# Kernel tuning notes

Hardware: AMD Instinct MI355X
Metric: run time of the kernel (lower is better)

The kernel has to match this reference:

```python
import jax, jax.numpy as jnp
import numpy as np

B, T, N, D, C = 32, 256, 256, 1024, 80
SIM_THRESH = 0.7
MAX_AGE = 10
W_SIM, W_IOU = 0.7, 0.3


def setup_inputs() -> dict:
    key = jax.random.key(0)
    ks = jax.random.split(key, 8)
    track_memory = jax.random.normal(ks[0], (B, T, D), jnp.float32)
    track_boxes = jax.random.uniform(ks[1], (B, T, 4), jnp.float32, 0.05, 0.95)
    track_active = jax.random.bernoulli(ks[2], 0.9, (B, T))
    track_age = jax.random.randint(ks[3], (B, T), 0, 5, jnp.int32)
    track_hits = jax.random.randint(ks[4], (B, T), 1, 10, jnp.int32)
    det_boxes = jax.random.uniform(ks[5], (B, N, 4), jnp.float32, 0.05, 0.95)
    # correlate detections with tracks so cosine similarity exceeds the
    # matching threshold for many pairs and the greedy loop does real work
    det_memory = track_memory + 0.3 * jax.random.normal(ks[6], (B, N, D), jnp.float32)
    class_logits = jax.random.normal(ks[7], (B, N, C), jnp.float32)
    return {
        'track_memory': track_memory, 'track_boxes': track_boxes,
        'track_active': track_active, 'track_age': track_age,
        'track_hits': track_hits, 'det_boxes': det_boxes,
        'det_memory': det_memory, 'class_logits': class_logits,
    }


def _normalize(x):
    # matches F.normalize(dim=-1): x / max(||x||, eps)
    n = jnp.linalg.norm(x, axis=-1, keepdims=True)
    return x / jnp.maximum(n, 1e-12)


def _iou_matrix(tb, db):
    # tb [T,4], db [N,4], boxes in (cx, cy, w, h) format -> IoU [T,N]
    t_x1, t_y1 = tb[:, 0] - tb[:, 2] / 2, tb[:, 1] - tb[:, 3] / 2
    t_x2, t_y2 = tb[:, 0] + tb[:, 2] / 2, tb[:, 1] + tb[:, 3] / 2
    d_x1, d_y1 = db[:, 0] - db[:, 2] / 2, db[:, 1] - db[:, 3] / 2
    d_x2, d_y2 = db[:, 0] + db[:, 2] / 2, db[:, 1] + db[:, 3] / 2
    iw = jnp.clip(jnp.minimum(t_x2[:, None], d_x2[None, :]) - jnp.maximum(t_x1[:, None], d_x1[None, :]), 0.0)
    ih = jnp.clip(jnp.minimum(t_y2[:, None], d_y2[None, :]) - jnp.maximum(t_y1[:, None], d_y1[None, :]), 0.0)
    inter = iw * ih
    union = (tb[:, 2] * tb[:, 3])[:, None] + (db[:, 2] * db[:, 3])[None, :] - inter
    return inter / (union + 1e-6)


def _greedy_match(Cmat):
    # sequential greedy argmax matching, as in the torch while-loop.
    # returns match_det [T]: detection index matched to each track, -1 if none.
    Tn, Nn = Cmat.shape

    def step(carry, _):
        Cm, match_det = carry
        flat = Cm.reshape(-1)
        idx = jnp.argmax(flat)
        val = flat[idx]
        ok = val >= SIM_THRESH
        t = idx // Nn
        d = idx % Nn
        match_det = jnp.where(ok, match_det.at[t].set(d.astype(jnp.int32)), match_det)
        Cm = jnp.where(ok, Cm.at[t, :].set(-1.0).at[:, d].set(-1.0), Cm)
        return (Cm, match_det), None

    init = (Cmat, jnp.full((Tn,), -1, jnp.int32))
    (_, match_det), _ = jax.lax.scan(step, init, None, length=min(Tn, Nn))
    return match_det


def reference(track_memory, track_boxes, track_active, track_age, track_hits,
              det_boxes, det_memory, class_logits):
    # detection scores (computed in torch update(); not used downstream)
    scores = jnp.max(jax.nn.softmax(class_logits, axis=-1), axis=-1)  # [B,N]

    def per_batch(tm, tb, ta, age, hits, db, dm):
        sim = _normalize(tm) @ _normalize(dm).T            # [T,N] cosine sim
        iou = _iou_matrix(tb, db)                          # [T,N]
        Cmat = W_SIM * sim + W_IOU * iou
        Cmat = jnp.where(ta[:, None], Cmat, -1.0)          # inactive rows -> -1
        match_det = _greedy_match(Cmat)                    # [T]
        matched = match_det >= 0
        d = jnp.clip(match_det, 0)
        new_mem = jnp.where(matched[:, None], dm[d], tm)
        new_box = jnp.where(matched[:, None], db[d], tb)
        new_hits = jnp.where(matched, hits + 1, hits)
        unmatched_active = ta & ~matched
        new_age = jnp.where(matched, 0, jnp.where(unmatched_active, age + 1, age))
        new_active = jnp.where(matched, True,
                               jnp.where(unmatched_active, new_age <= MAX_AGE, ta))
        return new_mem, new_box, new_active, new_age, new_hits, match_det

    new_mem, new_box, new_active, new_age, new_hits, match_det = jax.vmap(per_batch)(
        track_memory, track_boxes, track_active, track_age, track_hits,
        det_boxes, det_memory)
    return new_mem, new_box, new_active, new_age, new_hits, match_det, scores
```

## Files before the change

kernel.cpp:

```cpp
#include <hip/hip_runtime.h>
#include <math.h>

static constexpr int PB = 32, PT = 256, PN = 256, PD = 1024, PC = 80;
static constexpr int BCAP = 96;
static constexpr int CAP  = 256;
static constexpr int NT   = 16;

static constexpr size_t O_MEM   = 0;
static constexpr size_t O_BOX   = O_MEM   + (size_t)PB*PT*PD;
static constexpr size_t O_ACT   = O_BOX   + (size_t)PB*PT*4;
static constexpr size_t O_AGE   = O_ACT   + (size_t)PB*PT;
static constexpr size_t O_HITS  = O_AGE   + (size_t)PB*PT;
static constexpr size_t O_MATCH = O_HITS  + (size_t)PB*PT;
static constexpr size_t O_SCORE = O_MATCH + (size_t)PB*PT;

typedef __attribute__((ext_vector_type(8))) short short8;
typedef __attribute__((ext_vector_type(4))) float f32x4;


__device__ __forceinline__ unsigned ordbits(float f) {
    unsigned b = __float_as_uint(f);
    return (b & 0x80000000u) ? ~b : (b | 0x80000000u);
}
__device__ __forceinline__ unsigned short f2bf(float f) {
    unsigned u = __float_as_uint(f);
    unsigned r = u + 0x7fffu + ((u >> 16) & 1u);
    return (unsigned short)(r >> 16);
}
__device__ __forceinline__ short8 pack8(float4 lo, float4 hi) {
    union { unsigned u[4]; short8 s; } r;
    r.u[0] = f2bf(lo.x) | ((unsigned)f2bf(lo.y) << 16);
    r.u[1] = f2bf(lo.z) | ((unsigned)f2bf(lo.w) << 16);
    r.u[2] = f2bf(hi.x) | ((unsigned)f2bf(hi.y) << 16);
    r.u[3] = f2bf(hi.z) | ((unsigned)f2bf(hi.w) << 16);
    return r.s;
}

__device__ __forceinline__ float box_cost(float sim, float4 bt, float4 bd) {
    float tX1 = bt.x - bt.z*0.5f, tX2 = bt.x + bt.z*0.5f;
    float tY1 = bt.y - bt.w*0.5f, tY2 = bt.y + bt.w*0.5f;
    float dX1 = bd.x - bd.z*0.5f, dX2 = bd.x + bd.z*0.5f;
    float dY1 = bd.y - bd.w*0.5f, dY2 = bd.y + bd.w*0.5f;
    float iw = fmaxf(fminf(tX2, dX2) - fmaxf(tX1, dX1), 0.f);
    float ih = fmaxf(fminf(tY2, dY2) - fmaxf(tY1, dY1), 0.f);
    float inter = iw * ih;
    float iou = inter / (bt.z*bt.w + bd.z*bd.w - inter + 1e-6f);
    return 0.7f * sim + 0.3f * iou;
}

__global__ __launch_bounds__(512) void k_prep(
        const float* __restrict__ tm, const float* __restrict__ dm,
        const float* __restrict__ lg,
        short* __restrict__ abf, short* __restrict__ bbf,
        float* __restrict__ asums, float* __restrict__ bsums,
        float* __restrict__ ddots, float* __restrict__ out) {
    const int bx = blockIdx.x;
    const int tid = threadIdx.x;
    const int w = tid >> 6, lane = tid & 63;
    if (bx < PB * PT / 16) {
        const int m16 = lane & 15, quad = lane >> 4;
        const int row = bx * 16 + m16;
        const float* tp = tm + (size_t)row * PD;
        const float* dp = dm + (size_t)row * PD;
        const size_t fb = (size_t)bx * 32 * 512;
        float as = 0.f, bs = 0.f, dd = 0.f;
#pragma unroll
        for (int kq = 0; kq < 4; ++kq) {
            const int kk = w * 4 + kq;
            const int e = kk * 32 + quad * 8;
            float4 a0 = *(const float4*)(tp + e);
            float4 a1 = *(const float4*)(tp + e + 4);
            float4 d0 = *(const float4*)(dp + e);
            float4 d1 = *(const float4*)(dp + e + 4);
            as += a0.x*a0.x + a0.y*a0.y + a0.z*a0.z + a0.w*a0.w
                + a1.x*a1.x + a1.y*a1.y + a1.z*a1.z + a1.w*a1.w;
            bs += d0.x*d0.x + d0.y*d0.y + d0.z*d0.z + d0.w*d0.w
                + d1.x*d1.x + d1.y*d1.y + d1.z*d1.z + d1.w*d1.w;
            dd += a0.x*d0.x + a0.y*d0.y + a0.z*d0.z + a0.w*d0.w
                + a1.x*d1.x + a1.y*d1.y + a1.z*d1.z + a1.w*d1.w;
            *(short8*)(abf + fb + (size_t)kk * 512 + lane * 8) = pack8(a0, a1);
            *(short8*)(bbf + fb + (size_t)kk * 512 + lane * 8) = pack8(d0, d1);
        }
        as += __shfl_xor(as, 16); as += __shfl_xor(as, 32);
        bs += __shfl_xor(bs, 16); bs += __shfl_xor(bs, 32);
        dd += __shfl_xor(dd, 16); dd += __shfl_xor(dd, 32);
        __shared__ float red[3][8][16];
        if (quad == 0) { red[0][w][m16] = as; red[1][w][m16] = bs; red[2][w][m16] = dd; }
        __syncthreads();
        if (tid < 16) {
            int rg = bx * 16 + tid;
            float s0 = 0.f, s1 = 0.f, s2 = 0.f;
#pragma unroll
            for (int j = 0; j < 8; ++j) {
                s0 += red[0][j][tid]; s1 += red[1][j][tid]; s2 += red[2][j][tid];
            }
            asums[rg] = s0; bsums[rg] = s1; ddots[rg] = s2;
        }
    } else {
        int rowi = (bx - PB * PT / 16) * 8 + w;
        const float* p = lg + (size_t)rowi * PC;
        float x0 = p[lane];
        float x1 = (lane < PC - 64) ? p[64 + lane] : -INFINITY;
        float m = fmaxf(x0, x1);
#pragma unroll
        for (int o = 32; o > 0; o >>= 1) m = fmaxf(m, __shfl_down(m, o));
        m = __shfl(m, 0);
        float s = expf(x0 - m) + ((lane < PC - 64) ? expf(x1 - m) : 0.f);
#pragma unroll
        for (int o = 32; o > 0; o >>= 1) s += __shfl_down(s, o);
        if (lane == 0) out[O_SCORE + rowi] = 1.0f / s;
    }
}

__global__ __launch_bounds__(512) void k_sim(
        const short* __restrict__ abf, const short* __restrict__ bbf,
        const float* __restrict__ tb, const float* __restrict__ db,
        const unsigned* __restrict__ ta,
        const float* __restrict__ asums, const float* __restrict__ bsums,
        unsigned* __restrict__ cntblk, int* __restrict__ cand) {
    const int i = blockIdx.x;
    const int xcd = i & 7, j = i >> 3;
    const int b = xcd * 4 + (j >> 4);
    const int tile = j & 15;
    const int rowbase = (tile >> 2) * 64;
    const int colbase = (tile & 3) * 64;
    const int bid = b * NT + tile;
    const int tid = threadIdx.x;
    const int w = tid >> 6, lane = tid & 63;
    const int wm = w & 3, wn = w >> 2;
    const int m16 = lane & 15, quad = lane >> 4;

    __shared__ unsigned bcnt;
    __shared__ float ainv[64], binv[64];
    if (tid == 0) bcnt = 0u;
    if (tid < 64)
        ainv[tid] = 1.0f / fmaxf(sqrtf(asums[b * PT + rowbase + tid]), 1e-12f);
    else if (tid < 128)
        binv[tid - 64] = 1.0f / fmaxf(sqrtf(bsums[b * PN + colbase + tid - 64]), 1e-12f);

    const short8* A8 = (const short8*)abf;
    const short8* B8 = (const short8*)bbf;
    const size_t ab = ((size_t)(b * 16 + (rowbase >> 4) + wm)) * 2048 + lane;
    const size_t bbse = ((size_t)(b * 16 + (colbase >> 4) + wn * 2)) * 2048 + lane;

    f32x4 acc0 = (f32x4)0.f, acc1 = (f32x4)0.f;
    short8 av  = A8[ab];
    short8 b0v = B8[bbse];
    short8 b1v = B8[bbse + 2048];
#pragma unroll
    for (int kk = 0; kk < 31; ++kk) {
        const size_t o = (size_t)(kk + 1) * 64;
        short8 na  = A8[ab + o];
        short8 nb0 = B8[bbse + o];
        short8 nb1 = B8[bbse + o + 2048];
        acc0 = __builtin_amdgcn_mfma_f32_16x16x32_bf16(av, b0v, acc0, 0, 0, 0);
        acc1 = __builtin_amdgcn_mfma_f32_16x16x32_bf16(av, b1v, acc1, 0, 0, 0);
        av = na; b0v = nb0; b1v = nb1;
    }
    acc0 = __builtin_amdgcn_mfma_f32_16x16x32_bf16(av, b0v, acc0, 0, 0, 0);
    acc1 = __builtin_amdgcn_mfma_f32_16x16x32_bf16(av, b1v, acc1, 0, 0, 0);

    __syncthreads();

    float dx1[2], dy1[2], dx2[2], dy2[2], darea[2], dnv[2];
    int ng[2];
#pragma unroll
    for (int nj = 0; nj < 2; ++nj) {
        int cl = wn * 32 + nj * 16 + m16;
        ng[nj] = colbase + cl;
        dnv[nj] = binv[cl];
        float4 bx = *(const float4*)&db[((size_t)b * PN + ng[nj]) * 4];
        dx1[nj] = bx.x - bx.z * 0.5f; dx2[nj] = bx.x + bx.z * 0.5f;
        dy1[nj] = bx.y - bx.w * 0.5f; dy2[nj] = bx.y + bx.w * 0.5f;
        darea[nj] = bx.z * bx.w;
    }

#pragma unroll
    for (int r = 0; r < 4; ++r) {
        int tl = wm * 16 + quad * 4 + r;
        int tg = rowbase + tl;
        if (ta[b * PT + tg] == 0u) continue;
        float tnv = ainv[tl];
        float4 bx = *(const float4*)&tb[((size_t)b * PT + tg) * 4];
        float tX1 = bx.x - bx.z * 0.5f, tX2 = bx.x + bx.z * 0.5f;
        float tY1 = bx.y - bx.w * 0.5f, tY2 = bx.y + bx.w * 0.5f;
        float tA = bx.z * bx.w;
#pragma unroll
        for (int nj = 0; nj < 2; ++nj) {
            float sim = (nj == 0 ? acc0[r] : acc1[r]) * tnv * dnv[nj];
            float iw = fmaxf(fminf(tX2, dx2[nj]) - fmaxf(tX1, dx1[nj]), 0.f);
            float ih = fmaxf(fminf(tY2, dy2[nj]) - fmaxf(tY1, dy1[nj]), 0.f);
            float inter = iw * ih;
            float iou = inter / (tA + darea[nj] - inter + 1e-6f);
            float cost = 0.7f * sim + 0.3f * iou;
            if (cost >= 0.695f) {
                unsigned idx = atomicAdd(&bcnt, 1u);
                if (idx < BCAP) cand[bid * BCAP + idx] = (tg << 8) | ng[nj];
            }
        }
    }
    __syncthreads();
    if (tid == 0) cntblk[bid] = (bcnt > BCAP) ? BCAP : bcnt;
}

__global__ __launch_bounds__(512) void k_match(
        const float* __restrict__ tm, const float* __restrict__ dm,
        const float* __restrict__ tb, const float* __restrict__ db,
        const float* __restrict__ asums, const float* __restrict__ bsums,
        const float* __restrict__ ddots,
        const unsigned* __restrict__ cntblk, const int* __restrict__ cand,
        int* __restrict__ md) {
    const int b = blockIdx.x;
    const int tid = threadIdx.x;
    const int w = tid >> 6, lane = tid & 63;
    __shared__ int cnts[NT];
    __shared__ unsigned long long sel_key[CAP];
    __shared__ unsigned sel_cnt;
    __shared__ int odd_slot[64];
    __shared__ unsigned odd_cnt;
    __shared__ int rcnt[PT];
    __shared__ int ccnt[PN];
    __shared__ int conflict;

    if (tid == 0) { sel_cnt = 0u; odd_cnt = 0u; conflict = 0; }
    if (tid < NT) {
        int cj = (int)cntblk[b * NT + tid];
        cnts[tid] = (cj > BCAP) ? BCAP : cj;
    }
    if (tid < PT) { rcnt[tid] = 0; md[b * PT + tid] = -1; }
    if (tid < PN) ccnt[tid] = 0;
    __syncthreads();

    for (int u = tid; u < NT * BCAP; u += 512) {
        int j = u / BCAP, i = u - j * BCAP;
        if (i >= cnts[j]) continue;
        int gidx = (b * NT + j) * BCAP + i;
        int pair = cand[gidx];
        int t = pair >> 8, n = pair & 255;
        if (t == n) {
            float na  = asums[b * PT + t];
            float nb  = bsums[b * PN + n];
            float dot = ddots[b * PT + t];
            float sim = dot * (1.0f / fmaxf(sqrtf(na), 1e-12f))
                            * (1.0f / fmaxf(sqrtf(nb), 1e-12f));
            float4 bt = *(const float4*)&tb[((size_t)b * PT + t) * 4];
            float4 bd = *(const float4*)&db[((size_t)b * PN + n) * 4];
            float cost = box_cost(sim, bt, bd);
            if (cost >= 0.7f) {
                unsigned s = atomicAdd(&sel_cnt, 1u);
                if (s < CAP)
                    sel_key[s] = ((unsigned long long)ordbits(cost) << 16)
                               | (unsigned long long)(65535 - pair);
            }
        } else {
            unsigned oi = atomicAdd(&odd_cnt, 1u);
            if (oi < 64) odd_slot[oi] = gidx;
        }
    }
    __syncthreads();

    int nodd = (int)odd_cnt; if (nodd > 64) nodd = 64;
    for (int j = w; j < nodd; j += 8) {
        int pair = cand[odd_slot[j]];
        int t = pair >> 8, n = pair & 255;
        const float4* tr = (const float4*)(tm + ((size_t)b * PT + t) * PD);
        const float4* dr = (const float4*)(dm + ((size_t)b * PN + n) * PD);
        float dot = 0.f;
#pragma unroll
        for (int q = 0; q < 4; ++q) {
            float4 v = tr[lane + 64 * q];
            float4 u = dr[lane + 64 * q];
            dot += v.x*u.x + v.y*u.y + v.z*u.z + v.w*u.w;
        }
#pragma unroll
        for (int o = 1; o < 64; o <<= 1) dot += __shfl_xor(dot, o);
        if (lane == 0) {
            float na = asums[b * PT + t], nb = bsums[b * PN + n];
            float sim = dot * (1.0f / fmaxf(sqrtf(na), 1e-12f))
                            * (1.0f / fmaxf(sqrtf(nb), 1e-12f));
            float4 bt = *(const float4*)&tb[((size_t)b * PT + t) * 4];
            float4 bd = *(const float4*)&db[((size_t)b * PN + n) * 4];
            float cost = box_cost(sim, bt, bd);
            if (cost >= 0.7f) {
                unsigned s = atomicAdd(&sel_cnt, 1u);
                if (s < CAP)
                    sel_key[s] = ((unsigned long long)ordbits(cost) << 16)
                               | (unsigned long long)(65535 - pair);
            }
        }
    }
    __syncthreads();

    const unsigned ns = (sel_cnt > (unsigned)CAP) ? (unsigned)CAP : sel_cnt;
    for (unsigned s = tid; s < ns; s += 512) {
        int flat = 65535 - (int)(sel_key[s] & 0xFFFFull);
        if (atomicAdd(&rcnt[flat >> 8], 1) >= 1) conflict = 1;
        if (atomicAdd(&ccnt[flat & 255], 1) >= 1) conflict = 1;
    }
    __syncthreads();

    if (!conflict) {
        for (unsigned s = tid; s < ns; s += 512) {
            int flat = 65535 - (int)(sel_key[s] & 0xFFFFull);
            md[b * PT + (flat >> 8)] = flat & 255;
        }
        return;
    }

    if (w == 0) {
        unsigned long long k[4];
#pragma unroll
        for (int s = 0; s < 4; ++s) {
            unsigned idx = (unsigned)lane + 64u * s;
            k[s] = (idx < ns) ? sel_key[idx] : 0ull;
        }
        int mdv[4] = {-1, -1, -1, -1};
        for (int it = 0; it < PT; ++it) {
            unsigned long long m = k[0];
            if (k[1] > m) m = k[1];
            if (k[2] > m) m = k[2];
            if (k[3] > m) m = k[3];
#pragma unroll
            for (int o = 1; o < 64; o <<= 1) {
                unsigned long long s = __shfl_xor(m, o);
                if (s > m) m = s;
            }
            if (m == 0ull) break;
            int flat = 65535 - (int)(m & 0xFFFFull);
            int t = flat >> 8, d = flat & 255;
            if ((t & 63) == lane) mdv[t >> 6] = d;
#pragma unroll
            for (int s = 0; s < 4; ++s) {
                if (k[s]) {
                    int f2 = 65535 - (int)(k[s] & 0xFFFFull);
                    if ((f2 >> 8) == t || (f2 & 255) == d) k[s] = 0ull;
                }
            }
        }
#pragma unroll
        for (int s = 0; s < 4; ++s) md[b * PT + s * 64 + lane] = mdv[s];
    }
}

__global__ __launch_bounds__(256) void k_outsc(
        const float* __restrict__ tm, const float* __restrict__ tb,
        const unsigned* __restrict__ ta, const int* __restrict__ age,
        const int* __restrict__ hits, const float* __restrict__ db,
        const float* __restrict__ dm, const int* __restrict__ md,
        float* __restrict__ out) {
    const int w = threadIdx.x >> 6, lane = threadIdx.x & 63;
    int idx = blockIdx.x * 4 + w;
    int b = idx >> 8;
    int m = md[idx];
    bool matched = m >= 0;
    int d = matched ? m : 0;
    const float4* src = (const float4*)(matched ? dm + ((size_t)b * PN + d) * PD
                                                : tm + (size_t)idx * PD);
    float4* dst = (float4*)(out + O_MEM + (size_t)idx * PD);
#pragma unroll
    for (int q = 0; q < 4; ++q) dst[lane + 64 * q] = src[lane + 64 * q];
    if (lane < 4) {
        const float* sb = matched ? db + ((size_t)b * PN + d) * 4
                                  : tb + (size_t)idx * 4;
        out[O_BOX + (size_t)idx * 4 + lane] = sb[lane];
    }
    if (lane == 0) {
        bool tact = ta[idx] != 0u;
        int hh = hits[idx], ag = age[idx];
        int nh = matched ? hh + 1 : hh;
        bool unm = tact && !matched;
        int na = matched ? 0 : (unm ? ag + 1 : ag);
        bool nact = matched ? true : (unm ? (na <= 10) : tact);
        out[O_ACT   + idx] = nact ? 1.0f : 0.0f;
        out[O_AGE   + idx] = (float)na;
        out[O_HITS  + idx] = (float)nh;
        out[O_MATCH + idx] = (float)m;
    }
}

extern "C" void kernel_launch(void* const* d_in, const int* in_sizes, int n_in,
                              void* d_out, int out_size, void* d_ws, size_t ws_size,
                              hipStream_t stream) {
    const float*    tm   = (const float*)d_in[0];
    const float*    tb   = (const float*)d_in[1];
    const unsigned* ta   = (const unsigned*)d_in[2];
    const int*      age  = (const int*)d_in[3];
    const int*      hits = (const int*)d_in[4];
    const float*    db   = (const float*)d_in[5];
    const float*    dm   = (const float*)d_in[6];
    const float*    lg   = (const float*)d_in[7];
    float* out = (float*)d_out;

    char* ws = (char*)d_ws;
    short* abf   = (short*)ws;
    short* bbf   = abf + (size_t)PB * PT * PD;
    float* asums = (float*)(bbf + (size_t)PB * PN * PD);
    float* bsums = asums + PB * PT;
    float* ddots = bsums + PB * PN;
    unsigned* cntblk = (unsigned*)(ddots + PB * PT);
    int* cand = (int*)(cntblk + PB * NT);
    int* md   = cand + PB * NT * BCAP;

    k_prep <<<PB * PT / 16 + PB * PN / 8, 512, 0, stream>>>(
        tm, dm, lg, abf, bbf, asums, bsums, ddots, out);
    k_sim  <<<PB * NT, 512, 0, stream>>>(
        abf, bbf, tb, db, ta, asums, bsums, cntblk, cand);
    k_match<<<dim3(PB), 512, 0, stream>>>(
        tm, dm, tb, db, asums, bsums, ddots, cntblk, cand, md);
    k_outsc<<<PB * PT / 4, 256, 0, stream>>>(
        tm, tb, ta, age, hits, db, dm, md, out);
}
```

Before: 154.8 us.

## Fuse similarity and greedy-match kernels with last-block-done atomic counter

Merges the similarity/candidate kernel and the per-batch matching kernel into one launch. Each of the 16 tiles per batch bumps a per-batch done counter, and the last tile to finish runs the greedy match. This removes one kernel launch and its inter-kernel gap. In exchange it adds atomics and threadfences, raises the shared-memory footprint of every block, and puts the serial matching tail on a single late block per batch.

Result: slower. 168.2 us (+8.6%).

```diff
diff --git a/kernel.cpp b/kernel.cpp
--- a/kernel.cpp
+++ b/kernel.cpp
@@ -53,11 +53,13 @@
         const float* __restrict__ lg,
         short* __restrict__ abf, short* __restrict__ bbf,
         float* __restrict__ asums, float* __restrict__ bsums,
-        float* __restrict__ ddots, float* __restrict__ out) {
+        float* __restrict__ ddots, unsigned* __restrict__ done,
+        float* __restrict__ out) {
     const int bx = blockIdx.x;
     const int tid = threadIdx.x;
     const int w = tid >> 6, lane = tid & 63;
     if (bx < PB * PT / 16) {
+        if (bx == 0 && tid < PB) done[tid] = 0u;
         const int m16 = lane & 15, quad = lane >> 4;
         const int row = bx * 16 + m16;
         const float* tp = tm + (size_t)row * PD;
@@ -112,12 +114,15 @@
     }
 }
 
-__global__ __launch_bounds__(512) void k_sim(
+__global__ __launch_bounds__(512) void k_simmatch(
         const short* __restrict__ abf, const short* __restrict__ bbf,
+        const float* __restrict__ tm, const float* __restrict__ dm,
         const float* __restrict__ tb, const float* __restrict__ db,
         const unsigned* __restrict__ ta,
         const float* __restrict__ asums, const float* __restrict__ bsums,
-        unsigned* __restrict__ cntblk, int* __restrict__ cand) {
+        const float* __restrict__ ddots,
+        unsigned* __restrict__ cntblk, int* __restrict__ cand,
+        unsigned* __restrict__ done, int* __restrict__ md) {
     const int i = blockIdx.x;
     const int xcd = i & 7, j = i >> 3;
     const int b = xcd * 4 + (j >> 4);
@@ -195,24 +200,22 @@
             float cost = 0.7f * sim + 0.3f * iou;
             if (cost >= 0.695f) {
                 unsigned idx = atomicAdd(&bcnt, 1u);
-                if (idx < BCAP) cand[bid * BCAP + idx] = (tg << 8) | ng[nj];
-            }
-        }
-    }
-    __syncthreads();
-    if (tid == 0) cntblk[bid] = (bcnt > BCAP) ? BCAP : bcnt;
-}
-
-__global__ __launch_bounds__(512) void k_match(
-        const float* __restrict__ tm, const float* __restrict__ dm,
-        const float* __restrict__ tb, const float* __restrict__ db,
-        const float* __restrict__ asums, const float* __restrict__ bsums,
-        const float* __restrict__ ddots,
-        const unsigned* __restrict__ cntblk, const int* __restrict__ cand,
-        int* __restrict__ md) {
-    const int b = blockIdx.x;
-    const int tid = threadIdx.x;
-    const int w = tid >> 6, lane = tid & 63;
+                if (idx < BCAP)
+                    atomicExch(&cand[bid * BCAP + idx], (tg << 8) | ng[nj]);
+            }
+        }
+    }
+    __syncthreads();
+    __shared__ unsigned oldc;
+    if (tid == 0) {
+        atomicExch(&cntblk[bid], (bcnt > BCAP) ? BCAP : bcnt);
+        __threadfence();
+        oldc = atomicAdd(&done[b], 1u);
+    }
+    __syncthreads();
+    if (oldc != NT - 1) return;
+    __threadfence();
+
     __shared__ int cnts[NT];
     __shared__ unsigned long long sel_key[CAP];
     __shared__ unsigned sel_cnt;
@@ -224,7 +227,7 @@
 
     if (tid == 0) { sel_cnt = 0u; odd_cnt = 0u; conflict = 0; }
     if (tid < NT) {
-        int cj = (int)cntblk[b * NT + tid];
+        int cj = (int)atomicAdd(&cntblk[b * NT + tid], 0u);
         cnts[tid] = (cj > BCAP) ? BCAP : cj;
     }
     if (tid < PT) { rcnt[tid] = 0; md[b * PT + tid] = -1; }
@@ -232,10 +235,10 @@
     __syncthreads();
 
     for (int u = tid; u < NT * BCAP; u += 512) {
-        int j = u / BCAP, i = u - j * BCAP;
-        if (i >= cnts[j]) continue;
-        int gidx = (b * NT + j) * BCAP + i;
-        int pair = cand[gidx];
+        int jj = u / BCAP, ii = u - jj * BCAP;
+        if (ii >= cnts[jj]) continue;
+        int gidx = (b * NT + jj) * BCAP + ii;
+        int pair = atomicAdd(&cand[gidx], 0);
         int t = pair >> 8, n = pair & 255;
         if (t == n) {
             float na  = asums[b * PT + t];
@@ -254,14 +257,14 @@
             }
         } else {
             unsigned oi = atomicAdd(&odd_cnt, 1u);
-            if (oi < 64) odd_slot[oi] = gidx;
+            if (oi < 64) odd_slot[oi] = pair;
         }
     }
     __syncthreads();
 
     int nodd = (int)odd_cnt; if (nodd > 64) nodd = 64;
-    for (int j = w; j < nodd; j += 8) {
-        int pair = cand[odd_slot[j]];
+    for (int jj = w; jj < nodd; jj += 8) {
+        int pair = odd_slot[jj];
         int t = pair >> 8, n = pair & 255;
         const float4* tr = (const float4*)(tm + ((size_t)b * PT + t) * PD);
         const float4* dr = (const float4*)(dm + ((size_t)b * PN + n) * PD);
@@ -400,13 +403,12 @@
     unsigned* cntblk = (unsigned*)(ddots + PB * PT);
     int* cand = (int*)(cntblk + PB * NT);
     int* md   = cand + PB * NT * BCAP;
+    unsigned* done = (unsigned*)(md + PB * PT);
 
     k_prep <<<PB * PT / 16 + PB * PN / 8, 512, 0, stream>>>(
-        tm, dm, lg, abf, bbf, asums, bsums, ddots, out);
-    k_sim  <<<PB * NT, 512, 0, stream>>>(
-        abf, bbf, tb, db, ta, asums, bsums, cntblk, cand);
-    k_match<<<dim3(PB), 512, 0, stream>>>(
-        tm, dm, tb, db, asums, bsums, ddots, cntblk, cand, md);
+        tm, dm, lg, abf, bbf, asums, bsums, ddots, done, out);
+    k_simmatch<<<PB * NT, 512, 0, stream>>>(
+        abf, bbf, tm, dm, tb, db, ta, asums, bsums, ddots, cntblk, cand, done, md);
     k_outsc<<<PB * PT / 4, 256, 0, stream>>>(
         tm, tb, ta, age, hits, db, dm, md, out);
 }
```
